# Optimization experiments

Measured on AMD Instinct MI355X. Metric: run time of the kernel, lower is better.

## Reference

```python
import jax, jax.numpy as jnp
import numpy as np

VOCAB = 10000
X_DIM = 128
HID = 256


def setup_inputs() -> dict:
    key = jax.random.key(0)
    ks = jax.random.split(key, 8)
    B, S = 128, 50
    x = jax.random.randint(ks[0], (B, S), 0, VOCAB, dtype=jnp.int32).astype(jnp.int64)
    emb = jax.random.normal(ks[1], (VOCAB, X_DIM), dtype=jnp.float32) * 0.02
    # PyTorch nn.RNN params: W_ih [H, X], W_hh [H, H], b_ih [H], b_hh [H]
    W_ih = jax.random.normal(ks[2], (HID, X_DIM), dtype=jnp.float32) * (1.0 / np.sqrt(HID))
    W_hh = jax.random.normal(ks[3], (HID, HID), dtype=jnp.float32) * (1.0 / np.sqrt(HID))
    b_ih = jax.random.normal(ks[4], (HID,), dtype=jnp.float32) * 0.01
    b_hh = jax.random.normal(ks[5], (HID,), dtype=jnp.float32) * 0.01
    # nn.Linear: W_aff [V, H], b_aff [V]
    W_aff = jax.random.normal(ks[6], (VOCAB, HID), dtype=jnp.float32) * (1.0 / np.sqrt(HID))
    b_aff = jax.random.normal(ks[7], (VOCAB,), dtype=jnp.float32) * 0.01
    return {"x": x, "emb": emb, "W_ih": W_ih, "W_hh": W_hh,
            "b_ih": b_ih, "b_hh": b_hh, "W_aff": W_aff, "b_aff": b_aff}


def reference(x, emb, W_ih, W_hh, b_ih, b_hh, W_aff, b_aff):
    B, S = x.shape
    embs = emb[x]                                    # [B, S, X]
    # Precompute input projection for all timesteps (batched GEMM)
    xin = jnp.einsum('bsx,hx->bsh', embs, W_ih) + b_ih + b_hh  # [B, S, H]
    h0 = jnp.zeros((B, HID), dtype=embs.dtype)

    def step(h, xt):
        h = jnp.tanh(xt + h @ W_hh.T)
        return h, h

    _, hs = jax.lax.scan(step, h0, jnp.swapaxes(xin, 0, 1))  # hs: [S, B, H]
    hs = jnp.swapaxes(hs, 0, 1)                              # [B, S, H]
    ys = jnp.einsum('bsh,vh->bsv', hs, W_aff) + b_aff        # [B, S, V]
    return ys
```

## Files before the change

### kernel.cpp

```cpp
#include <hip/hip_runtime.h>
#include <hip/hip_bf16.h>
#include <stdint.h>

#define VOCAB 10000
#define XDIM 128
#define HID 256
#define BATCH 128
#define SEQ 50
#define ROWS (BATCH * SEQ)

#define BM 128
#define BN 128
#define BK 64
#define NTM 50
#define NTN 79

typedef __bf16 bf16x8 __attribute__((ext_vector_type(8)));
typedef float f32x4 __attribute__((ext_vector_type(4)));

__device__ __forceinline__ uint16_t f2bf(float f) {
    union { float f; uint32_t i; } v;
    v.f = f;
    uint32_t x = v.i;
    return (uint16_t)((x + 0x7fffu + ((x >> 16) & 1u)) >> 16);
}

__global__ __launch_bounds__(256) void k0_cast(
    const float* __restrict__ src, uint16_t* __restrict__ dst) {
    const int i = (blockIdx.x * 256 + threadIdx.x) * 8;
    float4 a = *(const float4*)(src + i);
    float4 b = *(const float4*)(src + i + 4);
    uint16_t t[8];
    t[0] = f2bf(a.x); t[1] = f2bf(a.y); t[2] = f2bf(a.z); t[3] = f2bf(a.w);
    t[4] = f2bf(b.x); t[5] = f2bf(b.y); t[6] = f2bf(b.z); t[7] = f2bf(b.w);
    *(uint4*)(dst + i) = *(const uint4*)t;
}

__global__ __launch_bounds__(256, 2) void k1_xin(
    const int* __restrict__ x, const float* __restrict__ emb,
    const float* __restrict__ Wih, const float* __restrict__ bih,
    const float* __restrict__ bhh, float* __restrict__ xin) {
    __shared__ __align__(16) float es[8][XDIM];
    const int r0 = blockIdx.x * 8;
    const int tid = threadIdx.x;

    {
        const int row = tid >> 5, c = tid & 31;
        const int tok = x[r0 + row];
        *(float4*)&es[row][c * 4] = *(const float4*)(emb + tok * XDIM + c * 4);
    }
    __syncthreads();

    const int j = tid;
    float wf[XDIM];
    const float4* wrow = (const float4*)(Wih + j * XDIM);
#pragma unroll
    for (int c = 0; c < 32; ++c) *(float4*)&wf[c * 4] = wrow[c];
    const float bias = bih[j] + bhh[j];

    float acc[8];
#pragma unroll
    for (int r = 0; r < 8; ++r) acc[r] = bias;
#pragma unroll
    for (int k4 = 0; k4 < 32; ++k4) {
#pragma unroll
        for (int r = 0; r < 8; ++r) {
            float4 e = *(const float4*)&es[r][k4 * 4];
            acc[r] += e.x * wf[k4 * 4 + 0] + e.y * wf[k4 * 4 + 1] +
                      e.z * wf[k4 * 4 + 2] + e.w * wf[k4 * 4 + 3];
        }
    }
#pragma unroll
    for (int r = 0; r < 8; ++r) xin[(r0 + r) * HID + j] = acc[r];
}

__global__ __launch_bounds__(256, 1) void k2_rnn(
    const float* __restrict__ xin, const float* __restrict__ Whh,
    uint16_t* __restrict__ hs) {
    __shared__ __align__(16) float hb[HID];
    const int b = blockIdx.x, j = threadIdx.x;

    float wh[HID];
    const float4* wrow = (const float4*)(Whh + j * HID);
#pragma unroll
    for (int c = 0; c < 64; ++c) *(float4*)&wh[c * 4] = wrow[c];

    hb[j] = 0.0f;
    __syncthreads();

    const float* xr = xin + b * SEQ * HID;
    uint16_t* hr = hs + b * SEQ * HID;

    for (int t = 0; t < SEQ; ++t) {
        float acc = xr[t * HID + j];
        const float4* h4 = (const float4*)hb;
        float a4[4] = {0.f, 0.f, 0.f, 0.f};
#pragma unroll
        for (int c = 0; c < 64; ++c) {
            float4 v = h4[c];
            a4[c & 3] += v.x * wh[4 * c + 0] + v.y * wh[4 * c + 1] +
                         v.z * wh[4 * c + 2] + v.w * wh[4 * c + 3];
        }
        acc += (a4[0] + a4[1]) + (a4[2] + a4[3]);
        float hn = tanhf(acc);
        __syncthreads();
        hb[j] = hn;
        hr[t * HID + j] = f2bf(hn);
        __syncthreads();
    }
}

__global__ __launch_bounds__(256, 2) void k3_gemm(
    const uint16_t* __restrict__ A,
    const uint16_t* __restrict__ Bw,
    const float* __restrict__ baff,
    float* __restrict__ out) {
    __shared__ __align__(16) uint16_t As[BM * BK];
    __shared__ __align__(16) uint16_t Bs[BN * BK];

    const int bid = blockIdx.x;
    const int bm = bid % NTM, bn = bid / NTM;
    const int m0 = bm * BM, n0 = bn * BN;
    const int tid = threadIdx.x;
    const int wv = tid >> 6, ln = tid & 63;
    const int wm = wv & 1, wn = wv >> 1;

    f32x4 acc[4][4];
#pragma unroll
    for (int i = 0; i < 4; ++i)
#pragma unroll
        for (int j = 0; j < 4; ++j) acc[i][j] = (f32x4)0.0f;

    const int lrow = ln >> 3;
    const int lcol = (ln & 7) * 8;

    for (int kt = 0; kt < 4; ++kt) {
        const int k0 = kt * BK;
#pragma unroll
        for (int i = 0; i < 4; ++i) {
            const int ci = wv * 4 + i;
            const uint16_t* g = A + (size_t)(m0 + ci * 8 + lrow) * HID + k0 + lcol;
            __builtin_amdgcn_global_load_lds(
                (const __attribute__((address_space(1))) void*)g,
                (__attribute__((address_space(3))) void*)(As + ci * 512), 16, 0, 0);
        }
#pragma unroll
        for (int i = 0; i < 4; ++i) {
            const int ci = wv * 4 + i;
            int n = n0 + ci * 8 + lrow;
            if (n > VOCAB - 1) n = VOCAB - 1;
            const uint16_t* g = Bw + (size_t)n * HID + k0 + lcol;
            __builtin_amdgcn_global_load_lds(
                (const __attribute__((address_space(1))) void*)g,
                (__attribute__((address_space(3))) void*)(Bs + ci * 512), 16, 0, 0);
        }
        __syncthreads();

#pragma unroll
        for (int kk = 0; kk < 2; ++kk) {
            const int krd = kk * 32 + (ln >> 4) * 8;
            bf16x8 af[4], bf[4];
#pragma unroll
            for (int tm = 0; tm < 4; ++tm)
                af[tm] = *(const bf16x8*)&As[(wm * 64 + tm * 16 + (ln & 15)) * BK + krd];
#pragma unroll
            for (int tn = 0; tn < 4; ++tn)
                bf[tn] = *(const bf16x8*)&Bs[(wn * 64 + tn * 16 + (ln & 15)) * BK + krd];
#pragma unroll
            for (int tm = 0; tm < 4; ++tm)
#pragma unroll
                for (int tn = 0; tn < 4; ++tn)
                    acc[tm][tn] = __builtin_amdgcn_mfma_f32_16x16x32_bf16(
                        af[tm], bf[tn], acc[tm][tn], 0, 0, 0);
        }
        __syncthreads();
    }

    float bias[4];
#pragma unroll
    for (int tn = 0; tn < 4; ++tn) {
        int n = n0 + wn * 64 + tn * 16 + (ln & 15);
        bias[tn] = baff[n > VOCAB - 1 ? VOCAB - 1 : n];
    }
#pragma unroll
    for (int tm = 0; tm < 4; ++tm) {
        const int mbase = m0 + wm * 64 + tm * 16 + (ln >> 4) * 4;
#pragma unroll
        for (int r = 0; r < 4; ++r) {
            float* orow = out + (size_t)(mbase + r) * VOCAB;
#pragma unroll
            for (int tn = 0; tn < 4; ++tn) {
                int n = n0 + wn * 64 + tn * 16 + (ln & 15);
                if (n < VOCAB) orow[n] = acc[tm][tn][r] + bias[tn];
            }
        }
    }
}

extern "C" void kernel_launch(void* const* d_in, const int* in_sizes, int n_in,
                              void* d_out, int out_size, void* d_ws, size_t ws_size,
                              hipStream_t stream) {
    const int* x = (const int*)d_in[0];
    const float* emb = (const float*)d_in[1];
    const float* Wih = (const float*)d_in[2];
    const float* Whh = (const float*)d_in[3];
    const float* bih = (const float*)d_in[4];
    const float* bhh = (const float*)d_in[5];
    const float* Waff = (const float*)d_in[6];
    const float* baff = (const float*)d_in[7];

    float* xin = (float*)d_ws;
    uint16_t* hsb = (uint16_t*)((char*)d_ws + (size_t)ROWS * HID * 4);
    uint16_t* Wb = hsb + (size_t)ROWS * HID;
    float* out = (float*)d_out;

    k0_cast<<<(VOCAB * HID) / (256 * 8), 256, 0, stream>>>(Waff, Wb);
    k1_xin<<<ROWS / 8, 256, 0, stream>>>(x, emb, Wih, bih, bhh, xin);
    k2_rnn<<<BATCH, 256, 0, stream>>>(xin, Whh, hsb);
    k3_gemm<<<NTM * NTN, 256, 0, stream>>>(hsb, Wb, baff, out);
}
```

Baseline: 431.1 us.

## Split RNN recurrence across two half-blocks and widen swizzled GEMM tiles

The recurrent kernel now runs 512 threads per batch row, each holding half of a W_hh row. The two partial dot products are combined through shared memory, which halves per-thread register weight storage and the serial dot-product length per step. The output GEMM widens its N tile to 256, so each wave computes 4x8 MFMA tiles. It also XOR-swizzles the LDS layout of the A and B tiles to avoid bank conflicts on fragment reads. The trade-off is higher accumulator register pressure and fewer GEMM blocks (2000 vs 3950), with more padding waste at the vocab edge (10240 vs 10112 columns).

```diff
diff --git a/kernel.cpp b/kernel.cpp
--- a/kernel.cpp
+++ b/kernel.cpp
@@ -10,10 +10,10 @@
 #define ROWS (BATCH * SEQ)
 
 #define BM 128
-#define BN 128
+#define BN 256
 #define BK 64
 #define NTM 50
-#define NTN 79
+#define NTN 40
 
 typedef __bf16 bf16x8 __attribute__((ext_vector_type(8)));
 typedef float f32x4 __attribute__((ext_vector_type(4)));
@@ -74,38 +74,46 @@
     for (int r = 0; r < 8; ++r) xin[(r0 + r) * HID + j] = acc[r];
 }
 
-__global__ __launch_bounds__(256, 1) void k2_rnn(
+__global__ __launch_bounds__(512, 2) void k2_rnn(
     const float* __restrict__ xin, const float* __restrict__ Whh,
     uint16_t* __restrict__ hs) {
     __shared__ __align__(16) float hb[HID];
-    const int b = blockIdx.x, j = threadIdx.x;
-
-    float wh[HID];
-    const float4* wrow = (const float4*)(Whh + j * HID);
-#pragma unroll
-    for (int c = 0; c < 64; ++c) *(float4*)&wh[c * 4] = wrow[c];
-
-    hb[j] = 0.0f;
+    __shared__ float ps[HID];
+    const int b = blockIdx.x;
+    const int j = threadIdx.x & 255;
+    const int half = threadIdx.x >> 8;
+
+    float wh[128];
+    const float4* wrow = (const float4*)(Whh + j * HID + half * 128);
+#pragma unroll
+    for (int c = 0; c < 32; ++c) *(float4*)&wh[c * 4] = wrow[c];
+
+    if (threadIdx.x < HID) hb[threadIdx.x] = 0.0f;
     __syncthreads();
 
     const float* xr = xin + b * SEQ * HID;
     uint16_t* hr = hs + b * SEQ * HID;
 
     for (int t = 0; t < SEQ; ++t) {
-        float acc = xr[t * HID + j];
-        const float4* h4 = (const float4*)hb;
-        float a4[4] = {0.f, 0.f, 0.f, 0.f};
-#pragma unroll
-        for (int c = 0; c < 64; ++c) {
+        const float xv = xr[t * HID + j];
+        const float4* h4 = (const float4*)(hb + half * 128);
+        float a0 = 0.f, a1 = 0.f, a2 = 0.f, a3 = 0.f;
+#pragma unroll
+        for (int c = 0; c < 32; ++c) {
             float4 v = h4[c];
-            a4[c & 3] += v.x * wh[4 * c + 0] + v.y * wh[4 * c + 1] +
-                         v.z * wh[4 * c + 2] + v.w * wh[4 * c + 3];
-        }
-        acc += (a4[0] + a4[1]) + (a4[2] + a4[3]);
-        float hn = tanhf(acc);
-        __syncthreads();
-        hb[j] = hn;
-        hr[t * HID + j] = f2bf(hn);
+            a0 += v.x * wh[c * 4 + 0];
+            a1 += v.y * wh[c * 4 + 1];
+            a2 += v.z * wh[c * 4 + 2];
+            a3 += v.w * wh[c * 4 + 3];
+        }
+        const float part = (a0 + a1) + (a2 + a3);
+        if (half) ps[j] = part;
+        __syncthreads();
+        if (!half) {
+            const float hn = tanhf(part + ps[j] + xv);
+            hb[j] = hn;
+            hr[t * HID + j] = f2bf(hn);
+        }
         __syncthreads();
     }
 }
@@ -124,32 +132,33 @@
     const int tid = threadIdx.x;
     const int wv = tid >> 6, ln = tid & 63;
     const int wm = wv & 1, wn = wv >> 1;
-
-    f32x4 acc[4][4];
+    const int quad = ln >> 4, l15 = ln & 15;
+
+    f32x4 acc[4][8];
 #pragma unroll
     for (int i = 0; i < 4; ++i)
 #pragma unroll
-        for (int j = 0; j < 4; ++j) acc[i][j] = (f32x4)0.0f;
+        for (int jj = 0; jj < 8; ++jj) acc[i][jj] = (f32x4)0.0f;
 
     const int lrow = ln >> 3;
-    const int lcol = (ln & 7) * 8;
+    const int gsw = ((ln & 7) ^ lrow) * 8;
 
     for (int kt = 0; kt < 4; ++kt) {
         const int k0 = kt * BK;
 #pragma unroll
         for (int i = 0; i < 4; ++i) {
             const int ci = wv * 4 + i;
-            const uint16_t* g = A + (size_t)(m0 + ci * 8 + lrow) * HID + k0 + lcol;
+            const uint16_t* g = A + (size_t)(m0 + ci * 8 + lrow) * HID + k0 + gsw;
             __builtin_amdgcn_global_load_lds(
                 (const __attribute__((address_space(1))) void*)g,
                 (__attribute__((address_space(3))) void*)(As + ci * 512), 16, 0, 0);
         }
 #pragma unroll
-        for (int i = 0; i < 4; ++i) {
-            const int ci = wv * 4 + i;
+        for (int i = 0; i < 8; ++i) {
+            const int ci = wv * 8 + i;
             int n = n0 + ci * 8 + lrow;
             if (n > VOCAB - 1) n = VOCAB - 1;
-            const uint16_t* g = Bw + (size_t)n * HID + k0 + lcol;
+            const uint16_t* g = Bw + (size_t)n * HID + k0 + gsw;
             __builtin_amdgcn_global_load_lds(
                 (const __attribute__((address_space(1))) void*)g,
                 (__attribute__((address_space(3))) void*)(Bs + ci * 512), 16, 0, 0);
@@ -158,39 +167,43 @@
 
 #pragma unroll
         for (int kk = 0; kk < 2; ++kk) {
-            const int krd = kk * 32 + (ln >> 4) * 8;
-            bf16x8 af[4], bf[4];
+            const int gk = kk * 4 + quad;
+            bf16x8 af[4], bf[8];
+#pragma unroll
+            for (int tm = 0; tm < 4; ++tm) {
+                const int R = wm * 64 + tm * 16 + l15;
+                af[tm] = *(const bf16x8*)&As[R * 64 + ((gk ^ (R & 7)) * 8)];
+            }
+#pragma unroll
+            for (int tn = 0; tn < 8; ++tn) {
+                const int R = wn * 128 + tn * 16 + l15;
+                bf[tn] = *(const bf16x8*)&Bs[R * 64 + ((gk ^ (R & 7)) * 8)];
+            }
 #pragma unroll
             for (int tm = 0; tm < 4; ++tm)
-                af[tm] = *(const bf16x8*)&As[(wm * 64 + tm * 16 + (ln & 15)) * BK + krd];
-#pragma unroll
-            for (int tn = 0; tn < 4; ++tn)
-                bf[tn] = *(const bf16x8*)&Bs[(wn * 64 + tn * 16 + (ln & 15)) * BK + krd];
-#pragma unroll
-            for (int tm = 0; tm < 4; ++tm)
-#pragma unroll
-                for (int tn = 0; tn < 4; ++tn)
+#pragma unroll
+                for (int tn = 0; tn < 8; ++tn)
                     acc[tm][tn] = __builtin_amdgcn_mfma_f32_16x16x32_bf16(
                         af[tm], bf[tn], acc[tm][tn], 0, 0, 0);
         }
         __syncthreads();
     }
 
-    float bias[4];
-#pragma unroll
-    for (int tn = 0; tn < 4; ++tn) {
-        int n = n0 + wn * 64 + tn * 16 + (ln & 15);
+    float bias[8];
+#pragma unroll
+    for (int tn = 0; tn < 8; ++tn) {
+        int n = n0 + wn * 128 + tn * 16 + l15;
         bias[tn] = baff[n > VOCAB - 1 ? VOCAB - 1 : n];
     }
 #pragma unroll
     for (int tm = 0; tm < 4; ++tm) {
-        const int mbase = m0 + wm * 64 + tm * 16 + (ln >> 4) * 4;
+        const int mbase = m0 + wm * 64 + tm * 16 + quad * 4;
 #pragma unroll
         for (int r = 0; r < 4; ++r) {
             float* orow = out + (size_t)(mbase + r) * VOCAB;
 #pragma unroll
-            for (int tn = 0; tn < 4; ++tn) {
-                int n = n0 + wn * 64 + tn * 16 + (ln & 15);
+            for (int tn = 0; tn < 8; ++tn) {
+                int n = n0 + wn * 128 + tn * 16 + l15;
                 if (n < VOCAB) orow[n] = acc[tm][tn][r] + bias[tn];
             }
         }
@@ -216,6 +229,6 @@
 
     k0_cast<<<(VOCAB * HID) / (256 * 8), 256, 0, stream>>>(Waff, Wb);
     k1_xin<<<ROWS / 8, 256, 0, stream>>>(x, emb, Wih, bih, bhh, xin);
-    k2_rnn<<<BATCH, 256, 0, stream>>>(xin, Whh, hsb);
+    k2_rnn<<<BATCH, 512, 0, stream>>>(xin, Whh, hsb);
     k3_gemm<<<NTM * NTN, 256, 0, stream>>>(hsb, Wb, baff, out);
 }
```

Result: faster. 382.7 us (-11.2%).
